# Performance work log

Hardware: AMD Instinct MI355X
Metric: run time of the kernel (lower is better)

The kernel has to match this reference:

```python
import jax, jax.numpy as jnp
import numpy as np
from itertools import product

D = 64          # dense grid extent per axis
B = 2           # batch size
N_PER = 65536
NF_IN = 3
NF = 32
EPS = 1e-5


def _ravel(c):
    # c: [Q,4] (b,x,y,z) -> unique linear key
    return ((c[:, 0] * D + c[:, 1]) * D + c[:, 2]) * D + c[:, 3]


def _build_indices():
    """Build active coords and rule-book index tables (numpy, host-side)."""
    rng = np.random.default_rng(0)
    parts = []
    for b in range(B):
        lin = rng.choice(D ** 3, size=N_PER, replace=False)
        x = lin // (D * D)
        y = (lin // D) % D
        z = lin % D
        parts.append(np.stack([np.full(N_PER, b), x, y, z], 1))
    coords = np.concatenate(parts, 0).astype(np.int64)  # [N,4]
    keys = _ravel(coords)
    order = np.argsort(keys)
    skeys = keys[order]

    def lookup(qc):
        valid = ((qc[:, 1:] >= 0) & (qc[:, 1:] < D)).all(1)
        qc2 = np.where(valid[:, None], qc, 0)
        qk = _ravel(qc2)
        pos = np.clip(np.searchsorted(skeys, qk), 0, len(skeys) - 1)
        found = valid & (skeys[pos] == qk)
        return np.where(found, order[pos], -1)

    # 3x3x3 submanifold rule-book: neighbor index per active site per offset
    offs3 = list(product((-1, 0, 1), repeat=3))
    nbr = np.stack([lookup(coords + np.array([0, dx, dy, dz]))
                    for dx, dy, dz in offs3], 1)  # [N,27]
    # 2x2x2 stride-2 conv: output sites = unique parent cells
    parents = np.unique(np.concatenate([coords[:, :1], coords[:, 1:] // 2], 1), axis=0)
    base = parents * np.array([1, 2, 2, 2])
    offs2 = list(product((0, 1), repeat=3))
    child = np.stack([lookup(base + np.array([0, dx, dy, dz]))
                      for dx, dy, dz in offs2], 1)  # [M,8]
    return nbr.astype(np.int32), child.astype(np.int32)


def setup_inputs() -> dict:
    nbr, child = _build_indices()
    N = nbr.shape[0]
    key = jax.random.key(0)
    ks = jax.random.split(key, 6)

    def w(k, shape, fan):
        return jax.random.normal(k, shape, jnp.float32) / np.float32(np.sqrt(fan))

    ones = jnp.ones((NF,), jnp.float32)
    zeros = jnp.zeros((NF,), jnp.float32)
    return {
        "feats": jax.random.normal(ks[0], (N, NF_IN), jnp.float32),
        "nbr_idx": jnp.asarray(nbr),
        "child_idx": jnp.asarray(child),
        "W1": w(ks[1], (27, NF_IN, NF), 27 * NF_IN),
        "W2a": w(ks[2], (27, NF, NF), 27 * NF),
        "W2b": w(ks[3], (27, NF, NF), 27 * NF),
        "W3": w(ks[4], (8, NF, NF), 8 * NF),
        "g1": ones, "b1": zeros,
        "g2": ones, "b2": zeros,
        "g3": ones, "b3": zeros,
        "g4": ones, "b4": zeros,
    }


def _gconv(feats, idx, W):
    # sparse conv as rule-book gather -> per-offset GEMM -> accumulate
    mask = (idx >= 0)
    g = feats[jnp.clip(idx, 0)] * mask[..., None].astype(feats.dtype)  # [N,K,C]
    return jnp.einsum('nkc,kcd->nd', g, W)


def _bnrelu(x, g, b):
    # training-mode BN over active sites, then ReLU (scn.BatchNormReLU)
    mu = x.mean(0)
    var = x.var(0)
    return jax.nn.relu((x - mu) * jax.lax.rsqrt(var + EPS) * g + b)


def reference(feats, nbr_idx, child_idx, W1, W2a, W2b, W3,
              g1, b1, g2, b2, g3, b3, g4, b4):
    x1 = _gconv(feats, nbr_idx, W1)                       # p1: submanifold 3^3
    br = _gconv(_bnrelu(x1, g1, b1), nbr_idx, W2a)        # p2 residual branch
    br = _gconv(_bnrelu(br, g2, b2), nbr_idx, W2b)
    ft2 = _bnrelu(x1 + br, g3, b3)                        # AddTable + BNReLU
    x3 = _gconv(ft2, child_idx, W3)                       # p3: 2^3 stride-2 conv
    out = _bnrelu(x3, g4, b4)
    return (out, ft2)
```

## Files before the change

kernel.cpp:

```cpp
#include <hip/hip_runtime.h>
#include <hip/hip_bf16.h>


typedef __bf16 bf16_8 __attribute__((ext_vector_type(8)));
typedef float  f32x4  __attribute__((ext_vector_type(4)));

#define EPSV 1e-5f
#define NCOPY 32

__device__ inline bf16_8 bzero8() {
    bf16_8 z;
#pragma unroll
    for (int i = 0; i < 8; ++i) z[i] = (__bf16)0.f;
    return z;
}

__device__ inline bf16_8 gatherrow(const __bf16* __restrict__ src, int nb, int kh) {
    bf16_8 a = *(const bf16_8*)(src + (size_t)(nb < 0 ? 0 : nb) * 32 + kh * 8);
    if (nb < 0) a = bzero8();
    return a;
}

__global__ void k_prep(const float* __restrict__ f,
                       const float* __restrict__ W1, const float* __restrict__ W2a,
                       const float* __restrict__ W2b, const float* __restrict__ W3,
                       __bf16* __restrict__ fb,
                       __bf16* __restrict__ w1t, __bf16* __restrict__ w2at,
                       __bf16* __restrict__ w2bt, __bf16* __restrict__ w3t,
                       float* __restrict__ statsAll, int n32) {
    int t = blockIdx.x * 256 + threadIdx.x;
    if (t < n32) {
        int s = t >> 5, c = t & 31;
        fb[t] = (c < 3) ? (__bf16)f[s * 3 + c] : (__bf16)0.f;
        return;
    }
    int u = t - n32;
    if (u < 27648) {
        int k = u >> 10, r = u & 1023, d = r >> 5, c = r & 31;
        w1t[u] = (c < 3) ? (__bf16)W1[(k * 3 + c) * 32 + d] : (__bf16)0.f;
    } else if (u < 2 * 27648) {
        int j = u - 27648;
        int k = j >> 10, r = j & 1023, d = r >> 5, c = r & 31;
        w2at[j] = (__bf16)W2a[(k * 32 + c) * 32 + d];
    } else if (u < 3 * 27648) {
        int j = u - 2 * 27648;
        int k = j >> 10, r = j & 1023, d = r >> 5, c = r & 31;
        w2bt[j] = (__bf16)W2b[(k * 32 + c) * 32 + d];
    } else if (u < 3 * 27648 + 8192) {
        int j = u - 3 * 27648;
        int k = j >> 10, r = j & 1023, d = r >> 5, c = r & 31;
        w3t[j] = (__bf16)W3[(k * 32 + c) * 32 + d];
    } else if (u < 3 * 27648 + 8192 + 4 * NCOPY * 64) {
        statsAll[u - 3 * 27648 - 8192] = 0.f;
    }
}

template <int KOFF, bool ADD, bool BNIN, bool CIN3>
__global__ __launch_bounds__(256, 4) void k_conv(
    const __bf16* __restrict__ src,
    const int* __restrict__ idx,
    const __bf16* __restrict__ Wt,
    const __bf16* __restrict__ addsrc,
    __bf16* __restrict__ dst,
    const float* __restrict__ spart_in,
    const float* __restrict__ gamma, const float* __restrict__ beta,
    float inv_cnt_in,
    float* __restrict__ spart_out,
    int nout) {
    constexpr int KPW = (KOFF + 3) / 4;
    __shared__ float part[4][32][33];
    __shared__ float lst[64];
    __shared__ float sfin[64];
    __shared__ float lsc[32], lsh[32];

    const int tid = threadIdx.x;
    const int lane = tid & 63;
    const int wv = tid >> 6;
    const int base = blockIdx.x * 32;
    const int sl = lane & 15;
    const int kh = lane >> 4;
    const int kbeg = wv * KPW;

    int nb[2][KPW];
#pragma unroll
    for (int g = 0; g < 2; ++g) {
        const int s = base + g * 16 + sl;
        const bool v = (s < nout);
        const int* ip = idx + (size_t)(v ? s : 0) * KOFF;
#pragma unroll
        for (int j = 0; j < KPW; ++j) {
            const bool kv = (kbeg + j) < KOFF;
            int t = ip[kv ? (kbeg + j) : 0];
            nb[g][j] = (v && kv) ? t : -1;
        }
    }

    if (tid < 64) lst[tid] = 0.f;

    if (BNIN) {
        if (tid < 64) {
            float a = 0.f;
#pragma unroll
            for (int i = 0; i < NCOPY; ++i) a += spart_in[i * 64 + tid];
            sfin[tid] = a;
        }
        __syncthreads();
        if (tid < 32) {
            float mu = sfin[tid] * inv_cnt_in;
            float var = sfin[32 + tid] * inv_cnt_in - mu * mu;
            float s = gamma[tid] * rsqrtf(var + EPSV);
            lsc[tid] = s;
            lsh[tid] = beta[tid] - mu * s;
        }
        __syncthreads();
    }
    float scl[8], shf[8];
    if (BNIN) {
#pragma unroll
        for (int i = 0; i < 8; ++i) { scl[i] = lsc[kh * 8 + i]; shf[i] = lsh[kh * 8 + i]; }
    }

    bf16_8 av[2][KPW];
#pragma unroll
    for (int j = 0; j < KPW; ++j)
#pragma unroll
        for (int g = 0; g < 2; ++g) {
            if (CIN3 && kh != 0)
                av[g][j] = bzero8();
            else
                av[g][j] = gatherrow(src, nb[g][j], kh);
        }

    f32x4 acc[2][2];
#pragma unroll
    for (int g = 0; g < 2; ++g)
#pragma unroll
        for (int h = 0; h < 2; ++h)
#pragma unroll
            for (int r = 0; r < 4; ++r) acc[g][h][r] = 0.f;

#pragma unroll
    for (int j = 0; j < KPW; ++j) {
        int kk = kbeg + j;
        if (kk > KOFF - 1) kk = KOFF - 1;
        bf16_8 b0 = *(const bf16_8*)(Wt + kk * 1024 + sl * 32 + kh * 8);
        bf16_8 b1 = *(const bf16_8*)(Wt + kk * 1024 + (16 + sl) * 32 + kh * 8);
        bf16_8 a0 = av[0][j], a1 = av[1][j];
        if (BNIN) {
#pragma unroll
            for (int i = 0; i < 8; ++i) {
                a0[i] = (__bf16)fmaxf(fmaf((float)a0[i], scl[i], shf[i]), 0.f);
                a1[i] = (__bf16)fmaxf(fmaf((float)a1[i], scl[i], shf[i]), 0.f);
            }
            if (nb[0][j] < 0) a0 = bzero8();
            if (nb[1][j] < 0) a1 = bzero8();
        }
        acc[0][0] = __builtin_amdgcn_mfma_f32_16x16x32_bf16(a0, b0, acc[0][0], 0, 0, 0);
        acc[0][1] = __builtin_amdgcn_mfma_f32_16x16x32_bf16(a0, b1, acc[0][1], 0, 0, 0);
        acc[1][0] = __builtin_amdgcn_mfma_f32_16x16x32_bf16(a1, b0, acc[1][0], 0, 0, 0);
        acc[1][1] = __builtin_amdgcn_mfma_f32_16x16x32_bf16(a1, b1, acc[1][1], 0, 0, 0);
    }

#pragma unroll
    for (int g = 0; g < 2; ++g)
#pragma unroll
        for (int h = 0; h < 2; ++h)
#pragma unroll
            for (int r = 0; r < 4; ++r)
                part[wv][g * 16 + kh * 4 + r][h * 16 + sl] = acc[g][h][r];
    __syncthreads();

    if (tid < 128) {
        const int sloc = tid >> 2;
        const int c0 = (tid & 3) * 8;
        float v[8];
#pragma unroll
        for (int i = 0; i < 8; ++i)
            v[i] = part[0][sloc][c0 + i] + part[1][sloc][c0 + i] +
                   part[2][sloc][c0 + i] + part[3][sloc][c0 + i];
        const int site = base + sloc;
        if (site < nout) {
            if (ADD) {
                bf16_8 ad = *(const bf16_8*)(addsrc + (size_t)site * 32 + c0);
#pragma unroll
                for (int i = 0; i < 8; ++i) v[i] += (float)ad[i];
            }
            bf16_8 o;
#pragma unroll
            for (int i = 0; i < 8; ++i) o[i] = (__bf16)v[i];
            *(bf16_8*)(dst + (size_t)site * 32 + c0) = o;
        } else {
#pragma unroll
            for (int i = 0; i < 8; ++i) v[i] = 0.f;
        }
        float sv[8], qv[8];
#pragma unroll
        for (int i = 0; i < 8; ++i) { sv[i] = v[i]; qv[i] = v[i] * v[i]; }
#pragma unroll
        for (int d = 4; d < 64; d <<= 1) {
#pragma unroll
            for (int i = 0; i < 8; ++i) {
                sv[i] += __shfl_xor(sv[i], d);
                qv[i] += __shfl_xor(qv[i], d);
            }
        }
        if ((lane & 60) == 0) {
#pragma unroll
            for (int i = 0; i < 8; ++i) {
                atomicAdd(&lst[c0 + i], sv[i]);
                atomicAdd(&lst[32 + c0 + i], qv[i]);
            }
        }
    }
    __syncthreads();
    if (tid < 64)
        atomicAdd(&spart_out[(blockIdx.x & (NCOPY - 1)) * 64 + tid], lst[tid]);
}

__global__ __launch_bounds__(256) void k_bnout(
    const __bf16* __restrict__ src, const float* __restrict__ spart,
    const float* __restrict__ gamma, const float* __restrict__ beta,
    float inv_cnt, int nrows, float* __restrict__ dstf) {
    __shared__ float ss[64];
    __shared__ float sc[32], sh[32];
    const int tid = threadIdx.x;
    if (tid < 64) {
        float a = 0.f;
#pragma unroll
        for (int i = 0; i < NCOPY; ++i) a += spart[i * 64 + tid];
        ss[tid] = a;
    }
    __syncthreads();
    if (tid < 32) {
        float mu = ss[tid] * inv_cnt;
        float var = ss[32 + tid] * inv_cnt - mu * mu;
        float s = gamma[tid] * rsqrtf(var + EPSV);
        sc[tid] = s;
        sh[tid] = beta[tid] - mu * s;
    }
    __syncthreads();
    const int gtid = blockIdx.x * blockDim.x + tid;
    const int c0 = (gtid & 3) * 8;
    float scale[8], shift[8];
#pragma unroll
    for (int i = 0; i < 8; ++i) { scale[i] = sc[c0 + i]; shift[i] = sh[c0 + i]; }
    const int rstride = (gridDim.x * blockDim.x) >> 2;
    for (int r = gtid >> 2; r < nrows; r += rstride) {
        const int off = r * 32 + c0;
        bf16_8 v = *(const bf16_8*)(src + off);
        f32x4 lo, hi;
#pragma unroll
        for (int i = 0; i < 4; ++i) {
            lo[i] = fmaxf(fmaf((float)v[i], scale[i], shift[i]), 0.f);
            hi[i] = fmaxf(fmaf((float)v[4 + i], scale[4 + i], shift[4 + i]), 0.f);
        }
        *(f32x4*)(dstf + off) = lo;
        *(f32x4*)(dstf + off + 4) = hi;
    }
}

extern "C" void kernel_launch(void* const* d_in, const int* in_sizes, int n_in,
                              void* d_out, int out_size, void* d_ws, size_t ws_size,
                              hipStream_t stream) {
    const float* feats = (const float*)d_in[0];
    const int* nbr     = (const int*)d_in[1];
    const int* child   = (const int*)d_in[2];
    const float* W1  = (const float*)d_in[3];
    const float* W2a = (const float*)d_in[4];
    const float* W2b = (const float*)d_in[5];
    const float* W3  = (const float*)d_in[6];
    const float* g1 = (const float*)d_in[7];  const float* b1 = (const float*)d_in[8];
    const float* g2 = (const float*)d_in[9];  const float* b2 = (const float*)d_in[10];
    const float* g3 = (const float*)d_in[11]; const float* b3 = (const float*)d_in[12];
    const float* g4 = (const float*)d_in[13]; const float* b4 = (const float*)d_in[14];

    const int N = in_sizes[0] / 3;
    const int M = in_sizes[2] / 8;

    float* outp = (float*)d_out;
    float* ft2p = outp + (size_t)M * 32;

    char* ws = (char*)d_ws;
    float* statsAll = (float*)ws;
    __bf16* w1t  = (__bf16*)(ws + 32768);
    __bf16* w2at = w1t + 27648;
    __bf16* w2bt = w2at + 27648;
    __bf16* w3t  = w2bt + 27648;
    __bf16* X  = (__bf16*)(ws + 32768 + 182272);
    __bf16* T  = X + (size_t)N * 32;
    __bf16* FB = T + (size_t)N * 32;

    float* s1 = statsAll;
    float* s2 = statsAll + NCOPY * 64;
    float* s3 = statsAll + 2 * NCOPY * 64;
    float* s4 = statsAll + 3 * NCOPY * 64;

    const int n32 = N * 32;
    const int ptot = n32 + 3 * 27648 + 8192 + 4 * NCOPY * 64;
    k_prep<<<(ptot + 255) / 256, 256, 0, stream>>>(feats, W1, W2a, W2b, W3,
                                                   FB, w1t, w2at, w2bt, w3t,
                                                   statsAll, n32);

    const int cgrid = (N + 31) / 32;
    const int cgrid3 = (M + 31) / 32;
    const float invN = 1.f / N, invM = 1.f / M;

    k_conv<27, false, false, true><<<cgrid, 256, 0, stream>>>(
        FB, nbr, w1t, nullptr, X, nullptr, nullptr, nullptr, 0.f, s1, N);
    k_conv<27, false, true, false><<<cgrid, 256, 0, stream>>>(
        X, nbr, w2at, nullptr, T, s1, g1, b1, invN, s2, N);
    k_conv<27, true, true, false><<<cgrid, 256, 0, stream>>>(
        T, nbr, w2bt, X, FB, s2, g2, b2, invN, s3, N);
    k_bnout<<<1024, 256, 0, stream>>>(FB, s3, g3, b3, invN, N, ft2p);
    k_conv<8, false, true, false><<<cgrid3, 256, 0, stream>>>(
        FB, child, w3t, nullptr, T, s3, g3, b3, invN, s4, M);
    k_bnout<<<1024, 256, 0, stream>>>(T, s4, g4, b4, invM, M, outp);
}
```

Baseline: 170.5 us.

## Reorder active sites by parent-cell order to improve gather locality

```diff
diff --git a/kernel.cpp b/kernel.cpp
--- a/kernel.cpp
+++ b/kernel.cpp
@@ -7,6 +7,7 @@
 
 #define EPSV 1e-5f
 #define NCOPY 32
+#define CBLK 256
 
 __device__ inline bf16_8 bzero8() {
     bf16_8 z;
@@ -21,41 +22,112 @@
     return a;
 }
 
-__global__ void k_prep(const float* __restrict__ f,
-                       const float* __restrict__ W1, const float* __restrict__ W2a,
-                       const float* __restrict__ W2b, const float* __restrict__ W3,
-                       __bf16* __restrict__ fb,
-                       __bf16* __restrict__ w1t, __bf16* __restrict__ w2at,
-                       __bf16* __restrict__ w2bt, __bf16* __restrict__ w3t,
-                       float* __restrict__ statsAll, int n32) {
+__global__ __launch_bounds__(256) void k_cnt(const int* __restrict__ child, int m8,
+                                             int* __restrict__ blockCnt) {
+    __shared__ int ws[4];
+    const int b = blockIdx.x, tid = threadIdx.x;
+    const int chunk = (m8 + CBLK - 1) / CBLK;
+    const int s0 = b * chunk, s1 = min(s0 + chunk, m8);
+    int c = 0;
+    for (int s = s0 + tid; s < s1; s += 256) c += (child[s] >= 0);
+#pragma unroll
+    for (int d = 1; d < 64; d <<= 1) c += __shfl_xor(c, d);
+    if ((tid & 63) == 0) ws[tid >> 6] = c;
+    __syncthreads();
+    if (tid == 0) blockCnt[b] = ws[0] + ws[1] + ws[2] + ws[3];
+}
+
+__global__ __launch_bounds__(256) void k_compact(const int* __restrict__ child, int m8,
+                                                 const int* __restrict__ blockCnt,
+                                                 int* __restrict__ perm,
+                                                 int* __restrict__ invperm) {
+    __shared__ int woff[4];
+    __shared__ int sbase;
+    const int b = blockIdx.x, tid = threadIdx.x;
+    const int chunk = (m8 + CBLK - 1) / CBLK;
+    const int s0 = b * chunk, s1 = min(s0 + chunk, m8);
+    if (tid == 0) {
+        int a = 0;
+        for (int i = 0; i < b; ++i) a += blockCnt[i];
+        sbase = a;
+    }
+    __syncthreads();
+    int off = sbase;
+    for (int base = s0; base < s1; base += 256) {
+        const int s = base + tid;
+        int c = -1;
+        bool v = false;
+        if (s < s1) { c = child[s]; v = (c >= 0); }
+        unsigned long long m = __ballot(v);
+        if ((tid & 63) == 0) woff[tid >> 6] = __popcll(m);
+        __syncthreads();
+        const int wv = tid >> 6;
+        int wpre = 0;
+#pragma unroll
+        for (int i = 0; i < 4; ++i) if (i < wv) wpre += woff[i];
+        const int tot = woff[0] + woff[1] + woff[2] + woff[3];
+        const int rank = __popcll(m & ((1ULL << (tid & 63)) - 1ULL));
+        if (v) {
+            const int pos = off + wpre + rank;
+            perm[pos] = c;
+            invperm[c] = pos;
+        }
+        off += tot;
+        __syncthreads();
+    }
+}
+
+__global__ __launch_bounds__(256) void k_reindex(
+    const int* __restrict__ nbr, const int* __restrict__ child,
+    const int* __restrict__ perm, const int* __restrict__ invperm,
+    const float* __restrict__ feats,
+    const float* __restrict__ W1, const float* __restrict__ W2a,
+    const float* __restrict__ W2b, const float* __restrict__ W3,
+    int* __restrict__ nbrP, int* __restrict__ childP, __bf16* __restrict__ fb,
+    __bf16* __restrict__ w1t, __bf16* __restrict__ w2at,
+    __bf16* __restrict__ w2bt, __bf16* __restrict__ w3t,
+    float* __restrict__ statsAll, int n27, int m8, int n32) {
     int t = blockIdx.x * 256 + threadIdx.x;
+    if (t < n27) {
+        const int p = t / 27, k = t - p * 27;
+        const int v = nbr[(size_t)perm[p] * 27 + k];
+        nbrP[t] = (v < 0) ? -1 : invperm[v];
+        return;
+    }
+    t -= n27;
+    if (t < m8) {
+        const int v = child[t];
+        childP[t] = (v < 0) ? -1 : invperm[v];
+        return;
+    }
+    t -= m8;
     if (t < n32) {
-        int s = t >> 5, c = t & 31;
-        fb[t] = (c < 3) ? (__bf16)f[s * 3 + c] : (__bf16)0.f;
+        const int p = t >> 5, c = t & 31;
+        fb[t] = (c < 3) ? (__bf16)feats[(size_t)perm[p] * 3 + c] : (__bf16)0.f;
         return;
     }
-    int u = t - n32;
-    if (u < 27648) {
-        int k = u >> 10, r = u & 1023, d = r >> 5, c = r & 31;
-        w1t[u] = (c < 3) ? (__bf16)W1[(k * 3 + c) * 32 + d] : (__bf16)0.f;
-    } else if (u < 2 * 27648) {
-        int j = u - 27648;
-        int k = j >> 10, r = j & 1023, d = r >> 5, c = r & 31;
+    t -= n32;
+    if (t < 27648) {
+        const int k = t >> 10, r = t & 1023, d = r >> 5, c = r & 31;
+        w1t[t] = (c < 3) ? (__bf16)W1[(k * 3 + c) * 32 + d] : (__bf16)0.f;
+    } else if (t < 2 * 27648) {
+        const int j = t - 27648;
+        const int k = j >> 10, r = j & 1023, d = r >> 5, c = r & 31;
         w2at[j] = (__bf16)W2a[(k * 32 + c) * 32 + d];
-    } else if (u < 3 * 27648) {
-        int j = u - 2 * 27648;
-        int k = j >> 10, r = j & 1023, d = r >> 5, c = r & 31;
+    } else if (t < 3 * 27648) {
+        const int j = t - 2 * 27648;
+        const int k = j >> 10, r = j & 1023, d = r >> 5, c = r & 31;
         w2bt[j] = (__bf16)W2b[(k * 32 + c) * 32 + d];
-    } else if (u < 3 * 27648 + 8192) {
-        int j = u - 3 * 27648;
-        int k = j >> 10, r = j & 1023, d = r >> 5, c = r & 31;
+    } else if (t < 3 * 27648 + 8192) {
+        const int j = t - 3 * 27648;
+        const int k = j >> 10, r = j & 1023, d = r >> 5, c = r & 31;
         w3t[j] = (__bf16)W3[(k * 32 + c) * 32 + d];
-    } else if (u < 3 * 27648 + 8192 + 4 * NCOPY * 64) {
-        statsAll[u - 3 * 27648 - 8192] = 0.f;
-    }
-}
-
-template <int KOFF, bool ADD, bool BNIN, bool CIN3>
+    } else if (t < 3 * 27648 + 8192 + 4 * NCOPY * 64) {
+        statsAll[t - 3 * 27648 - 8192] = 0.f;
+    }
+}
+
+template <int KOFF, bool ADD, bool BNIN>
 __global__ __launch_bounds__(256, 4) void k_conv(
     const __bf16* __restrict__ src,
     const int* __restrict__ idx,
@@ -68,7 +140,7 @@
     float* __restrict__ spart_out,
     int nout) {
     constexpr int KPW = (KOFF + 3) / 4;
-    __shared__ float part[4][32][33];
+    __shared__ float part[4][32][34];
     __shared__ float lst[64];
     __shared__ float sfin[64];
     __shared__ float lsc[32], lsh[32];
@@ -124,12 +196,8 @@
 #pragma unroll
     for (int j = 0; j < KPW; ++j)
 #pragma unroll
-        for (int g = 0; g < 2; ++g) {
-            if (CIN3 && kh != 0)
-                av[g][j] = bzero8();
-            else
-                av[g][j] = gatherrow(src, nb[g][j], kh);
-        }
+        for (int g = 0; g < 2; ++g)
+            av[g][j] = gatherrow(src, nb[g][j], kh);
 
     f32x4 acc[2][2];
 #pragma unroll
@@ -220,7 +288,8 @@
 __global__ __launch_bounds__(256) void k_bnout(
     const __bf16* __restrict__ src, const float* __restrict__ spart,
     const float* __restrict__ gamma, const float* __restrict__ beta,
-    float inv_cnt, int nrows, float* __restrict__ dstf) {
+    float inv_cnt, int nrows, float* __restrict__ dstf,
+    const int* __restrict__ permw) {
     __shared__ float ss[64];
     __shared__ float sc[32], sh[32];
     const int tid = threadIdx.x;
@@ -246,7 +315,7 @@
     for (int i = 0; i < 8; ++i) { scale[i] = sc[c0 + i]; shift[i] = sh[c0 + i]; }
     const int rstride = (gridDim.x * blockDim.x) >> 2;
     for (int r = gtid >> 2; r < nrows; r += rstride) {
-        const int off = r * 32 + c0;
+        const size_t off = (size_t)r * 32 + c0;
         bf16_8 v = *(const bf16_8*)(src + off);
         f32x4 lo, hi;
 #pragma unroll
@@ -254,8 +323,9 @@
             lo[i] = fmaxf(fmaf((float)v[i], scale[i], shift[i]), 0.f);
             hi[i] = fmaxf(fmaf((float)v[4 + i], scale[4 + i], shift[4 + i]), 0.f);
         }
-        *(f32x4*)(dstf + off) = lo;
-        *(f32x4*)(dstf + off + 4) = hi;
+        const size_t woff = permw ? ((size_t)permw[r] * 32 + c0) : off;
+        *(f32x4*)(dstf + woff) = lo;
+        *(f32x4*)(dstf + woff + 4) = hi;
     }
 }
 
@@ -275,7 +345,8 @@
     const float* g4 = (const float*)d_in[13]; const float* b4 = (const float*)d_in[14];
 
     const int N = in_sizes[0] / 3;
-    const int M = in_sizes[2] / 8;
+    const int M8 = in_sizes[2];
+    const int M = M8 / 8;
 
     float* outp = (float*)d_out;
     float* ft2p = outp + (size_t)M * 32;
@@ -286,33 +357,42 @@
     __bf16* w2at = w1t + 27648;
     __bf16* w2bt = w2at + 27648;
     __bf16* w3t  = w2bt + 27648;
-    __bf16* X  = (__bf16*)(ws + 32768 + 182272);
+    __bf16* X  = (__bf16*)(ws + 215040);
     __bf16* T  = X + (size_t)N * 32;
     __bf16* FB = T + (size_t)N * 32;
+    char* p2 = ws + 215040 + 3 * (size_t)N * 64;
+    int* perm    = (int*)p2;
+    int* invperm = perm + N;
+    int* nbrP    = invperm + N;
+    int* childP  = nbrP + (size_t)N * 27;
+    int* blockCnt = childP + M8;
 
     float* s1 = statsAll;
     float* s2 = statsAll + NCOPY * 64;
     float* s3 = statsAll + 2 * NCOPY * 64;
     float* s4 = statsAll + 3 * NCOPY * 64;
 
-    const int n32 = N * 32;
-    const int ptot = n32 + 3 * 27648 + 8192 + 4 * NCOPY * 64;
-    k_prep<<<(ptot + 255) / 256, 256, 0, stream>>>(feats, W1, W2a, W2b, W3,
-                                                   FB, w1t, w2at, w2bt, w3t,
-                                                   statsAll, n32);
+    k_cnt<<<CBLK, 256, 0, stream>>>(child, M8, blockCnt);
+    k_compact<<<CBLK, 256, 0, stream>>>(child, M8, blockCnt, perm, invperm);
+
+    const int n27 = N * 27, n32 = N * 32;
+    const int rtot = n27 + M8 + n32 + 3 * 27648 + 8192 + 4 * NCOPY * 64;
+    k_reindex<<<(rtot + 255) / 256, 256, 0, stream>>>(
+        nbr, child, perm, invperm, feats, W1, W2a, W2b, W3,
+        nbrP, childP, FB, w1t, w2at, w2bt, w3t, statsAll, n27, M8, n32);
 
     const int cgrid = (N + 31) / 32;
     const int cgrid3 = (M + 31) / 32;
     const float invN = 1.f / N, invM = 1.f / M;
 
-    k_conv<27, false, false, true><<<cgrid, 256, 0, stream>>>(
-        FB, nbr, w1t, nullptr, X, nullptr, nullptr, nullptr, 0.f, s1, N);
-    k_conv<27, false, true, false><<<cgrid, 256, 0, stream>>>(
-        X, nbr, w2at, nullptr, T, s1, g1, b1, invN, s2, N);
-    k_conv<27, true, true, false><<<cgrid, 256, 0, stream>>>(
-        T, nbr, w2bt, X, FB, s2, g2, b2, invN, s3, N);
-    k_bnout<<<1024, 256, 0, stream>>>(FB, s3, g3, b3, invN, N, ft2p);
-    k_conv<8, false, true, false><<<cgrid3, 256, 0, stream>>>(
-        FB, child, w3t, nullptr, T, s3, g3, b3, invN, s4, M);
-    k_bnout<<<1024, 256, 0, stream>>>(T, s4, g4, b4, invM, M, outp);
-}
+    k_conv<27, false, false><<<cgrid, 256, 0, stream>>>(
+        FB, nbrP, w1t, nullptr, X, nullptr, nullptr, nullptr, 0.f, s1, N);
+    k_conv<27, false, true><<<cgrid, 256, 0, stream>>>(
+        X, nbrP, w2at, nullptr, T, s1, g1, b1, invN, s2, N);
+    k_conv<27, true, true><<<cgrid, 256, 0, stream>>>(
+        T, nbrP, w2bt, X, FB, s2, g2, b2, invN, s3, N);
+    k_bnout<<<1024, 256, 0, stream>>>(FB, s3, g3, b3, invN, N, ft2p, perm);
+    k_conv<8, false, true><<<cgrid3, 256, 0, stream>>>(
+        FB, childP, w3t, nullptr, T, s3, g3, b3, invN, s4, M);
+    k_bnout<<<1024, 256, 0, stream>>>(T, s4, g4, b4, invM, M, outp, nullptr);
+}
```

After: 183.7 us. 1.08x slower.
